# Performance work log

Measured on AMD Instinct MI355X. Metric: run time of the kernel, lower is better.

## Reference

```python
import jax, jax.numpy as jnp
import numpy as np

B, S, H, DK, DV, D = 1024, 8, 16, 32, 32, 512


def setup_inputs() -> dict:
    key = jax.random.key(0)
    ks = jax.random.split(key, 12)
    s = 1.0 / np.sqrt(D)
    return {
        "Q": jax.random.normal(ks[0], (B, S, D), jnp.float32),
        "K": jax.random.normal(ks[1], (B, S, D), jnp.float32),
        "V": jax.random.normal(ks[2], (B, S, D), jnp.float32),
        "attn_mask": jax.random.bernoulli(ks[3], 0.2, (B, S, S)),
        "hyper": jax.random.normal(ks[4], (B, H * S * DK), jnp.float32),
        "Wq": jax.random.normal(ks[5], (H * DK, D), jnp.float32) * s,
        "bq": jnp.zeros((H * DK,), jnp.float32),
        "Wk": jax.random.normal(ks[6], (H * DK, D), jnp.float32) * s,
        "bk": jnp.zeros((H * DK,), jnp.float32),
        "Wv": jax.random.normal(ks[7], (H * DV, D), jnp.float32) * s,
        "bv": jnp.zeros((H * DV,), jnp.float32),
        "Wo": jax.random.normal(ks[8], (D, H * DV), jnp.float32) * s,
        "bo": jnp.zeros((D,), jnp.float32),
        "ln_g": jnp.ones((D,), jnp.float32),
        "ln_b": jnp.zeros((D,), jnp.float32),
    }


def reference(Q, K, V, attn_mask, hyper, Wq, bq, Wk, bk, Wv, bv, Wo, bo, ln_g, ln_b):
    # QKV projections -> [B, H, S, dk]
    q = (Q @ Wq.T + bq).reshape(B, S, H, DK).transpose(0, 2, 1, 3)
    k = (K @ Wk.T + bk).reshape(B, S, H, DK).transpose(0, 2, 1, 3)
    v = (V @ Wv.T + bv).reshape(B, S, H, DV).transpose(0, 2, 1, 3)
    # scaled dot-product attention with mask
    scores = jnp.einsum('bhqd,bhkd->bhqk', q, k) / np.sqrt(DK).astype(np.float32)
    scores = jnp.where(attn_mask[:, None, :, :], -1e9, scores)
    weights = jax.nn.softmax(scores, axis=-1)
    # hyper-gated AV
    context = jnp.einsum('bhqk,bhkd->bhqd', weights, v) * hyper.reshape(B, H, S, DK)
    context = context.transpose(0, 2, 1, 3).reshape(B, S, H * DV)
    # output projection + residual layernorm (eps=1e-5)
    out = context @ Wo.T + bo + Q
    mu = out.mean(axis=-1, keepdims=True)
    var = out.var(axis=-1, keepdims=True)
    out = (out - mu) * jax.lax.rsqrt(var + 1e-5) * ln_g + ln_b
    return (out, weights)
```

## Files before the change

kernel.cpp:

```cpp
#include <hip/hip_runtime.h>
#include <hip/hip_bf16.h>
#include <cstdint>

#define NB 1024
#define ND 512
#define NM 8192

typedef __attribute__((ext_vector_type(8))) short short8;
typedef __attribute__((ext_vector_type(8))) __bf16 bf16x8;
typedef __attribute__((ext_vector_type(4))) float f32x4;
typedef __attribute__((ext_vector_type(4))) unsigned short ushort4v;

__device__ __forceinline__ unsigned short f2bf(float f) {
  uint32_t x = __builtin_bit_cast(uint32_t, f);
  x += 0x7fffu + ((x >> 16) & 1u);
  return (unsigned short)(x >> 16);
}
__device__ __forceinline__ float bf2f(unsigned short u) {
  return __builtin_bit_cast(float, (uint32_t)u << 16);
}
__device__ __forceinline__ f32x4 mfma16(short8 a, short8 b, f32x4 c) {
  return __builtin_amdgcn_mfma_f32_16x16x32_bf16(
      __builtin_bit_cast(bf16x8, a), __builtin_bit_cast(bf16x8, b), c, 0, 0, 0);
}

__global__ __launch_bounds__(256) void convert_w(
    const float* __restrict__ Wq, const float* __restrict__ Wk,
    const float* __restrict__ Wv, const float* __restrict__ Wo,
    unsigned short* __restrict__ Wqb, unsigned short* __restrict__ Wkb,
    unsigned short* __restrict__ Wvb, unsigned short* __restrict__ Wob) {
  const int idx = blockIdx.x * 256 + threadIdx.x;
  const int sel = idx >> 15, o = (idx & 32767) * 8;
  const float* src = sel == 0 ? Wq : sel == 1 ? Wk : sel == 2 ? Wv : Wo;
  unsigned short* dst = sel == 0 ? Wqb : sel == 1 ? Wkb : sel == 2 ? Wvb : Wob;
  const float4 a = ((const float4*)(src + o))[0];
  const float4 b = ((const float4*)(src + o))[1];
  short8 r;
  r[0] = (short)f2bf(a.x); r[1] = (short)f2bf(a.y);
  r[2] = (short)f2bf(a.z); r[3] = (short)f2bf(a.w);
  r[4] = (short)f2bf(b.x); r[5] = (short)f2bf(b.y);
  r[6] = (short)f2bf(b.z); r[7] = (short)f2bf(b.w);
  *(short8*)(dst + o) = r;
}

template <bool A_F32, int MODE>
__device__ __forceinline__ void gemm_tile(const void* __restrict__ A,
                                          const unsigned short* __restrict__ W,
                                          const float* __restrict__ bias,
                                          const float* __restrict__ resid,
                                          void* __restrict__ C, int mBase, int nBase) {
  __shared__ unsigned short As[128 * 64];
  __shared__ unsigned short Bs[128 * 64];
  const int tid = threadIdx.x;
  const int lane = tid & 63, wid = tid >> 6;
  const int wm = wid >> 2, wn = wid & 3;
  const int l15 = lane & 15, l4 = lane >> 4;
  f32x4 acc[4][2] = {};

  for (int kt = 0; kt < 8; ++kt) {
    const int kBase = kt * 64;
#pragma unroll
    for (int i = 0; i < 2; ++i) {
      const int Lb = i * 8192 + tid * 16;
      const int r = Lb >> 7;
      const int ce = (Lb & 127) >> 1;
      const int P = Lb ^ ((r & 7) << 4);
      short8 av;
      if (A_F32) {
        const float* src = (const float*)A + (size_t)(mBase + r) * ND + kBase + ce;
        const float4 a = ((const float4*)src)[0];
        const float4 b = ((const float4*)src)[1];
        av[0] = (short)f2bf(a.x); av[1] = (short)f2bf(a.y);
        av[2] = (short)f2bf(a.z); av[3] = (short)f2bf(a.w);
        av[4] = (short)f2bf(b.x); av[5] = (short)f2bf(b.y);
        av[6] = (short)f2bf(b.z); av[7] = (short)f2bf(b.w);
      } else {
        av = *(const short8*)((const unsigned short*)A +
                              (size_t)(mBase + r) * ND + kBase + ce);
      }
      const short8 wv = *(const short8*)(W + (size_t)(nBase + r) * ND + kBase + ce);
      *(short8*)((char*)As + P) = av;
      *(short8*)((char*)Bs + P) = wv;
    }
    __syncthreads();
#pragma unroll
    for (int kk = 0; kk < 2; ++kk) {
      short8 af[4], bf4[2];
#pragma unroll
      for (int m = 0; m < 4; ++m) {
        const int r = wm * 64 + m * 16 + l15;
        const int Lb = r * 128 + kk * 64 + l4 * 16;
        af[m] = *(const short8*)((char*)As + (Lb ^ ((r & 7) << 4)));
      }
#pragma unroll
      for (int n = 0; n < 2; ++n) {
        const int r = wn * 32 + n * 16 + l15;
        const int Lb = r * 128 + kk * 64 + l4 * 16;
        bf4[n] = *(const short8*)((char*)Bs + (Lb ^ ((r & 7) << 4)));
      }
#pragma unroll
      for (int m = 0; m < 4; ++m)
#pragma unroll
        for (int n = 0; n < 2; ++n)
          acc[m][n] = mfma16(af[m], bf4[n], acc[m][n]);
    }
    __syncthreads();
  }

#pragma unroll
  for (int m = 0; m < 4; ++m)
#pragma unroll
    for (int n = 0; n < 2; ++n) {
      const int gn = nBase + wn * 32 + n * 16 + l15;
      const float bb = bias ? bias[gn] : 0.f;
#pragma unroll
      for (int r4 = 0; r4 < 4; ++r4) {
        const int gm = mBase + wm * 64 + m * 16 + l4 * 4 + r4;
        float val = acc[m][n][r4] + bb;
        if (MODE == 0) {
          ((unsigned short*)C)[(size_t)gm * ND + gn] = f2bf(val);
        } else {
          val += resid[(size_t)gm * ND + gn];
          ((float*)C)[(size_t)gm * ND + gn] = val;
        }
      }
    }
}

__global__ __launch_bounds__(512) void gemm_qkv(
    const float* __restrict__ Q, const float* __restrict__ K,
    const float* __restrict__ V, const unsigned short* __restrict__ Wqb,
    const unsigned short* __restrict__ Wkb, const unsigned short* __restrict__ Wvb,
    const float* __restrict__ bq, const float* __restrict__ bk,
    const float* __restrict__ bv, unsigned short* __restrict__ qo,
    unsigned short* __restrict__ ko, unsigned short* __restrict__ vo) {
  const int bid = blockIdx.x;
  const int lid = (bid & 7) * 96 + (bid >> 3);
  const int by = lid / 12, bx = lid % 12;
  const int seg = bx >> 2, nloc = bx & 3;
  const float* A = seg == 0 ? Q : seg == 1 ? K : V;
  const unsigned short* W = seg == 0 ? Wqb : seg == 1 ? Wkb : Wvb;
  const float* bias = seg == 0 ? bq : seg == 1 ? bk : bv;
  unsigned short* C = seg == 0 ? qo : seg == 1 ? ko : vo;
  gemm_tile<true, 0>(A, W, bias, nullptr, C, by * 128, nloc * 128);
}

__global__ __launch_bounds__(512) void gemm_wo(const unsigned short* __restrict__ ctx,
                                               const unsigned short* __restrict__ Wob,
                                               const float* __restrict__ bo,
                                               const float* __restrict__ Qres,
                                               float* __restrict__ out) {
  const int bid = blockIdx.x;
  const int lid = (bid & 7) * 32 + (bid >> 3);
  const int by = lid >> 2, bx = lid & 3;
  gemm_tile<false, 1>(ctx, Wob, bo, Qres, out, by * 128, bx * 128);
}

__global__ __launch_bounds__(256) void attn_kernel(
    const unsigned short* __restrict__ q, const unsigned short* __restrict__ k,
    const unsigned short* __restrict__ v, const int* __restrict__ mask,
    const float* __restrict__ hyper, float* __restrict__ wout,
    unsigned short* __restrict__ ctx) {
  const int tid = threadIdx.x;
  const int wid = tid >> 6, lane = tid & 63;
  const int t = blockIdx.x * 4 + wid;
  const int b = t >> 4, h = t & 15;
  const int i = lane >> 3, j = lane & 7;

  const unsigned short* qrow = q + (size_t)(b * 8 + i) * ND + h * 32;
  const unsigned short* krow = k + (size_t)(b * 8 + j) * ND + h * 32;
  float dot = 0.f;
#pragma unroll
  for (int c = 0; c < 4; ++c) {
    const short8 qv = ((const short8*)qrow)[c];
    const short8 kv = ((const short8*)krow)[c];
#pragma unroll
    for (int e = 0; e < 8; ++e)
      dot += bf2f((unsigned short)qv[e]) * bf2f((unsigned short)kv[e]);
  }
  float score = dot * 0.17677669529663687f;
  if (mask[b * 64 + i * 8 + j]) score = -1e9f;

  float mx = score;
#pragma unroll
  for (int o = 4; o; o >>= 1) mx = fmaxf(mx, __shfl_xor(mx, o, 8));
  const float e = __expf(score - mx);
  float sm = e;
#pragma unroll
  for (int o = 4; o; o >>= 1) sm += __shfl_xor(sm, o, 8);
  const float w = e / sm;
  wout[(size_t)t * 64 + lane] = w;

  const int d0 = (lane & 7) * 4;
  float c0 = 0, c1 = 0, c2 = 0, c3 = 0;
#pragma unroll
  for (int jj = 0; jj < 8; ++jj) {
    const float wj = __shfl(w, jj, 8);
    const ushort4v vv = *(const ushort4v*)(v + (size_t)(b * 8 + jj) * ND + h * 32 + d0);
    c0 += wj * bf2f(vv[0]); c1 += wj * bf2f(vv[1]);
    c2 += wj * bf2f(vv[2]); c3 += wj * bf2f(vv[3]);
  }
  const float4 hv = *(const float4*)(hyper + (size_t)b * 4096 + h * 256 + i * 32 + d0);
  ushort4v co;
  co[0] = f2bf(c0 * hv.x); co[1] = f2bf(c1 * hv.y);
  co[2] = f2bf(c2 * hv.z); co[3] = f2bf(c3 * hv.w);
  *(ushort4v*)(ctx + (size_t)(b * 8 + i) * ND + h * 32 + d0) = co;
}

__global__ __launch_bounds__(256) void ln_kernel(float* __restrict__ io,
                                                 const float* __restrict__ g,
                                                 const float* __restrict__ be) {
  const int tid = threadIdx.x, wid = tid >> 6, lane = tid & 63;
  const size_t row = (size_t)blockIdx.x * 4 + wid;
  float* prow = io + row * ND + lane * 8;
  float4 x0 = ((float4*)prow)[0], x1 = ((float4*)prow)[1];
  float s = x0.x + x0.y + x0.z + x0.w + x1.x + x1.y + x1.z + x1.w;
  float sq = x0.x * x0.x + x0.y * x0.y + x0.z * x0.z + x0.w * x0.w +
             x1.x * x1.x + x1.y * x1.y + x1.z * x1.z + x1.w * x1.w;
#pragma unroll
  for (int o = 32; o; o >>= 1) {
    s += __shfl_xor(s, o, 64);
    sq += __shfl_xor(sq, o, 64);
  }
  const float mu = s * (1.f / 512.f);
  const float inv = rsqrtf(sq * (1.f / 512.f) - mu * mu + 1e-5f);
  const float4 g0 = ((const float4*)(g + lane * 8))[0];
  const float4 g1 = ((const float4*)(g + lane * 8))[1];
  const float4 e0 = ((const float4*)(be + lane * 8))[0];
  const float4 e1 = ((const float4*)(be + lane * 8))[1];
  float4 o0, o1;
  o0.x = (x0.x - mu) * inv * g0.x + e0.x; o0.y = (x0.y - mu) * inv * g0.y + e0.y;
  o0.z = (x0.z - mu) * inv * g0.z + e0.z; o0.w = (x0.w - mu) * inv * g0.w + e0.w;
  o1.x = (x1.x - mu) * inv * g1.x + e1.x; o1.y = (x1.y - mu) * inv * g1.y + e1.y;
  o1.z = (x1.z - mu) * inv * g1.z + e1.z; o1.w = (x1.w - mu) * inv * g1.w + e1.w;
  ((float4*)prow)[0] = o0;
  ((float4*)prow)[1] = o1;
}

extern "C" void kernel_launch(void* const* d_in, const int* in_sizes, int n_in,
                              void* d_out, int out_size, void* d_ws, size_t ws_size,
                              hipStream_t stream) {
  const float* Q = (const float*)d_in[0];
  const float* K = (const float*)d_in[1];
  const float* V = (const float*)d_in[2];
  const int* msk = (const int*)d_in[3];
  const float* hyper = (const float*)d_in[4];
  const float* Wq = (const float*)d_in[5];
  const float* bq = (const float*)d_in[6];
  const float* Wk = (const float*)d_in[7];
  const float* bk = (const float*)d_in[8];
  const float* Wv = (const float*)d_in[9];
  const float* bv = (const float*)d_in[10];
  const float* Wo = (const float*)d_in[11];
  const float* bo = (const float*)d_in[12];
  const float* lg = (const float*)d_in[13];
  const float* lb = (const float*)d_in[14];

  float* out = (float*)d_out;
  float* wout = out + (size_t)NM * ND;

  const size_t MAT = (size_t)NM * ND;
  unsigned short* qb = (unsigned short*)d_ws;
  unsigned short* kb = qb + MAT;
  unsigned short* vb = kb + MAT;
  unsigned short* ctxb = vb + MAT;
  unsigned short* Wqb = ctxb + MAT;
  unsigned short* Wkb = Wqb + (size_t)ND * ND;
  unsigned short* Wvb = Wkb + (size_t)ND * ND;
  unsigned short* Wob = Wvb + (size_t)ND * ND;

  convert_w<<<512, 256, 0, stream>>>(Wq, Wk, Wv, Wo, Wqb, Wkb, Wvb, Wob);
  gemm_qkv<<<768, 512, 0, stream>>>(Q, K, V, Wqb, Wkb, Wvb,
                                    bq, bk, bv, qb, kb, vb);
  attn_kernel<<<4096, 256, 0, stream>>>(qb, kb, vb, msk, hyper, wout, ctxb);
  gemm_wo<<<256, 512, 0, stream>>>(ctxb, Wob, bo, Q, out);
  ln_kernel<<<2048, 256, 0, stream>>>(out, lg, lb);
}
```

Measured before the change: 74.64 us.

## Prefetch next K-tile into registers during MFMA compute in GEMM tiles

```diff
diff --git a/kernel.cpp b/kernel.cpp
--- a/kernel.cpp
+++ b/kernel.cpp
@@ -43,6 +43,9 @@
   *(short8*)(dst + o) = r;
 }
 
+struct StageF32 { float4 a[4]; short8 w[2]; };
+struct StageBF  { short8 ab[2]; short8 w[2]; };
+
 template <bool A_F32, int MODE>
 __device__ __forceinline__ void gemm_tile(const void* __restrict__ A,
                                           const unsigned short* __restrict__ W,
@@ -55,34 +58,58 @@
   const int lane = tid & 63, wid = tid >> 6;
   const int wm = wid >> 2, wn = wid & 3;
   const int l15 = lane & 15, l4 = lane >> 4;
+  const int Lb0 = tid * 16, Lb1 = 8192 + tid * 16;
+  const int r0 = Lb0 >> 7, c0 = (Lb0 & 127) >> 1, P0 = Lb0 ^ ((r0 & 7) << 4);
+  const int r1 = Lb1 >> 7, c1 = (Lb1 & 127) >> 1, P1 = Lb1 ^ ((r1 & 7) << 4);
+
   f32x4 acc[4][2] = {};
-
+  StageF32 sf, nf;
+  StageBF sb, nb;
+
+  auto issue = [&](int kt, StageF32& f, StageBF& bfs) {
+    const int kBase = kt * 64;
+    if (A_F32) {
+      const float* s0 = (const float*)A + (size_t)(mBase + r0) * ND + kBase + c0;
+      const float* s1 = (const float*)A + (size_t)(mBase + r1) * ND + kBase + c1;
+      f.a[0] = ((const float4*)s0)[0]; f.a[1] = ((const float4*)s0)[1];
+      f.a[2] = ((const float4*)s1)[0]; f.a[3] = ((const float4*)s1)[1];
+      f.w[0] = *(const short8*)(W + (size_t)(nBase + r0) * ND + kBase + c0);
+      f.w[1] = *(const short8*)(W + (size_t)(nBase + r1) * ND + kBase + c1);
+    } else {
+      bfs.ab[0] = *(const short8*)((const unsigned short*)A + (size_t)(mBase + r0) * ND + kBase + c0);
+      bfs.ab[1] = *(const short8*)((const unsigned short*)A + (size_t)(mBase + r1) * ND + kBase + c1);
+      bfs.w[0] = *(const short8*)(W + (size_t)(nBase + r0) * ND + kBase + c0);
+      bfs.w[1] = *(const short8*)(W + (size_t)(nBase + r1) * ND + kBase + c1);
+    }
+  };
+  auto write_lds = [&](StageF32& f, StageBF& bfs) {
+    short8 av0, av1;
+    if (A_F32) {
+      av0[0] = (short)f2bf(f.a[0].x); av0[1] = (short)f2bf(f.a[0].y);
+      av0[2] = (short)f2bf(f.a[0].z); av0[3] = (short)f2bf(f.a[0].w);
+      av0[4] = (short)f2bf(f.a[1].x); av0[5] = (short)f2bf(f.a[1].y);
+      av0[6] = (short)f2bf(f.a[1].z); av0[7] = (short)f2bf(f.a[1].w);
+      av1[0] = (short)f2bf(f.a[2].x); av1[1] = (short)f2bf(f.a[2].y);
+      av1[2] = (short)f2bf(f.a[2].z); av1[3] = (short)f2bf(f.a[2].w);
+      av1[4] = (short)f2bf(f.a[3].x); av1[5] = (short)f2bf(f.a[3].y);
+      av1[6] = (short)f2bf(f.a[3].z); av1[7] = (short)f2bf(f.a[3].w);
+      *(short8*)((char*)As + P0) = av0;
+      *(short8*)((char*)As + P1) = av1;
+      *(short8*)((char*)Bs + P0) = f.w[0];
+      *(short8*)((char*)Bs + P1) = f.w[1];
+    } else {
+      *(short8*)((char*)As + P0) = bfs.ab[0];
+      *(short8*)((char*)As + P1) = bfs.ab[1];
+      *(short8*)((char*)Bs + P0) = bfs.w[0];
+      *(short8*)((char*)Bs + P1) = bfs.w[1];
+    }
+  };
+
+  issue(0, sf, sb);
   for (int kt = 0; kt < 8; ++kt) {
-    const int kBase = kt * 64;
-#pragma unroll
-    for (int i = 0; i < 2; ++i) {
-      const int Lb = i * 8192 + tid * 16;
-      const int r = Lb >> 7;
-      const int ce = (Lb & 127) >> 1;
-      const int P = Lb ^ ((r & 7) << 4);
-      short8 av;
-      if (A_F32) {
-        const float* src = (const float*)A + (size_t)(mBase + r) * ND + kBase + ce;
-        const float4 a = ((const float4*)src)[0];
-        const float4 b = ((const float4*)src)[1];
-        av[0] = (short)f2bf(a.x); av[1] = (short)f2bf(a.y);
-        av[2] = (short)f2bf(a.z); av[3] = (short)f2bf(a.w);
-        av[4] = (short)f2bf(b.x); av[5] = (short)f2bf(b.y);
-        av[6] = (short)f2bf(b.z); av[7] = (short)f2bf(b.w);
-      } else {
-        av = *(const short8*)((const unsigned short*)A +
-                              (size_t)(mBase + r) * ND + kBase + ce);
-      }
-      const short8 wv = *(const short8*)(W + (size_t)(nBase + r) * ND + kBase + ce);
-      *(short8*)((char*)As + P) = av;
-      *(short8*)((char*)Bs + P) = wv;
-    }
+    write_lds(sf, sb);
     __syncthreads();
+    if (kt < 7) issue(kt + 1, nf, nb);
 #pragma unroll
     for (int kk = 0; kk < 2; ++kk) {
       short8 af[4], bf4[2];
@@ -105,6 +132,8 @@
           acc[m][n] = mfma16(af[m], bf4[n], acc[m][n]);
     }
     __syncthreads();
+    sf = nf;
+    sb = nb;
   }
 
 #pragma unroll
@@ -127,7 +156,7 @@
     }
 }
 
-__global__ __launch_bounds__(512) void gemm_qkv(
+__global__ __launch_bounds__(512, 6) void gemm_qkv(
     const float* __restrict__ Q, const float* __restrict__ K,
     const float* __restrict__ V, const unsigned short* __restrict__ Wqb,
     const unsigned short* __restrict__ Wkb, const unsigned short* __restrict__ Wvb,
@@ -145,11 +174,11 @@
   gemm_tile<true, 0>(A, W, bias, nullptr, C, by * 128, nloc * 128);
 }
 
-__global__ __launch_bounds__(512) void gemm_wo(const unsigned short* __restrict__ ctx,
-                                               const unsigned short* __restrict__ Wob,
-                                               const float* __restrict__ bo,
-                                               const float* __restrict__ Qres,
-                                               float* __restrict__ out) {
+__global__ __launch_bounds__(512, 2) void gemm_wo(const unsigned short* __restrict__ ctx,
+                                                  const unsigned short* __restrict__ Wob,
+                                                  const float* __restrict__ bo,
+                                                  const float* __restrict__ Qres,
+                                                  float* __restrict__ out) {
   const int bid = blockIdx.x;
   const int lid = (bid & 7) * 32 + (bid >> 3);
   const int by = lid >> 2, bx = lid & 3;
```

Measured after the change: 72.97 us. -2.2%, faster.

## Use 256-wide K tiles with register-prefetched double staging in projection GEMMs

Applied to the files above, without the earlier changes.

```diff
diff --git a/kernel.cpp b/kernel.cpp
--- a/kernel.cpp
+++ b/kernel.cpp
@@ -44,58 +44,74 @@
 }
 
 template <bool A_F32, int MODE>
-__device__ __forceinline__ void gemm_tile(const void* __restrict__ A,
-                                          const unsigned short* __restrict__ W,
-                                          const float* __restrict__ bias,
-                                          const float* __restrict__ resid,
-                                          void* __restrict__ C, int mBase, int nBase) {
-  __shared__ unsigned short As[128 * 64];
-  __shared__ unsigned short Bs[128 * 64];
+__device__ __forceinline__ void gemm_big(const void* __restrict__ A,
+                                         const unsigned short* __restrict__ W,
+                                         const float* __restrict__ bias,
+                                         const float* __restrict__ resid,
+                                         void* __restrict__ C, int mBase, int nBase) {
+  __shared__ unsigned short As[128 * 256];
+  __shared__ unsigned short Bs[128 * 256];
   const int tid = threadIdx.x;
   const int lane = tid & 63, wid = tid >> 6;
   const int wm = wid >> 2, wn = wid & 3;
   const int l15 = lane & 15, l4 = lane >> 4;
+
   f32x4 acc[4][2] = {};
-
-  for (int kt = 0; kt < 8; ++kt) {
-    const int kBase = kt * 64;
-#pragma unroll
-    for (int i = 0; i < 2; ++i) {
-      const int Lb = i * 8192 + tid * 16;
-      const int r = Lb >> 7;
-      const int ce = (Lb & 127) >> 1;
+  float4 sa[16];
+  short8 sab[8];
+  short8 sw[8];
+
+  auto issue = [&](int kt) {
+    const int kBase = kt * 256;
+#pragma unroll
+    for (int j = 0; j < 8; ++j) {
+      const int Lb = j * 8192 + tid * 16;
+      const int r = Lb >> 9, ce = (Lb & 511) >> 1;
+      if (A_F32) {
+        const float* s = (const float*)A + (size_t)(mBase + r) * ND + kBase + ce;
+        sa[j * 2] = ((const float4*)s)[0];
+        sa[j * 2 + 1] = ((const float4*)s)[1];
+      } else {
+        sab[j] = *(const short8*)((const unsigned short*)A +
+                                  (size_t)(mBase + r) * ND + kBase + ce);
+      }
+      sw[j] = *(const short8*)(W + (size_t)(nBase + r) * ND + kBase + ce);
+    }
+  };
+  auto write_lds = [&]() {
+#pragma unroll
+    for (int j = 0; j < 8; ++j) {
+      const int Lb = j * 8192 + tid * 16;
+      const int r = Lb >> 9;
       const int P = Lb ^ ((r & 7) << 4);
-      short8 av;
       if (A_F32) {
-        const float* src = (const float*)A + (size_t)(mBase + r) * ND + kBase + ce;
-        const float4 a = ((const float4*)src)[0];
-        const float4 b = ((const float4*)src)[1];
-        av[0] = (short)f2bf(a.x); av[1] = (short)f2bf(a.y);
-        av[2] = (short)f2bf(a.z); av[3] = (short)f2bf(a.w);
-        av[4] = (short)f2bf(b.x); av[5] = (short)f2bf(b.y);
-        av[6] = (short)f2bf(b.z); av[7] = (short)f2bf(b.w);
+        short8 av;
+        const float4 a0 = sa[j * 2], a1 = sa[j * 2 + 1];
+        av[0] = (short)f2bf(a0.x); av[1] = (short)f2bf(a0.y);
+        av[2] = (short)f2bf(a0.z); av[3] = (short)f2bf(a0.w);
+        av[4] = (short)f2bf(a1.x); av[5] = (short)f2bf(a1.y);
+        av[6] = (short)f2bf(a1.z); av[7] = (short)f2bf(a1.w);
+        *(short8*)((char*)As + P) = av;
       } else {
-        av = *(const short8*)((const unsigned short*)A +
-                              (size_t)(mBase + r) * ND + kBase + ce);
-      }
-      const short8 wv = *(const short8*)(W + (size_t)(nBase + r) * ND + kBase + ce);
-      *(short8*)((char*)As + P) = av;
-      *(short8*)((char*)Bs + P) = wv;
+        *(short8*)((char*)As + P) = sab[j];
+      }
+      *(short8*)((char*)Bs + P) = sw[j];
     }
-    __syncthreads();
-#pragma unroll
-    for (int kk = 0; kk < 2; ++kk) {
+  };
+  auto compute = [&]() {
+#pragma unroll
+    for (int kk = 0; kk < 8; ++kk) {
       short8 af[4], bf4[2];
 #pragma unroll
       for (int m = 0; m < 4; ++m) {
         const int r = wm * 64 + m * 16 + l15;
-        const int Lb = r * 128 + kk * 64 + l4 * 16;
+        const int Lb = r * 512 + kk * 64 + l4 * 16;
         af[m] = *(const short8*)((char*)As + (Lb ^ ((r & 7) << 4)));
       }
 #pragma unroll
       for (int n = 0; n < 2; ++n) {
         const int r = wn * 32 + n * 16 + l15;
-        const int Lb = r * 128 + kk * 64 + l4 * 16;
+        const int Lb = r * 512 + kk * 64 + l4 * 16;
         bf4[n] = *(const short8*)((char*)Bs + (Lb ^ ((r & 7) << 4)));
       }
 #pragma unroll
@@ -104,8 +120,18 @@
         for (int n = 0; n < 2; ++n)
           acc[m][n] = mfma16(af[m], bf4[n], acc[m][n]);
     }
-    __syncthreads();
-  }
+  };
+
+  issue(0);
+  write_lds();
+  __syncthreads();
+  issue(1);
+  __builtin_amdgcn_sched_barrier(0);
+  compute();
+  __syncthreads();
+  write_lds();
+  __syncthreads();
+  compute();
 
 #pragma unroll
   for (int m = 0; m < 4; ++m)
@@ -127,7 +153,7 @@
     }
 }
 
-__global__ __launch_bounds__(512) void gemm_qkv(
+__global__ __launch_bounds__(512, 2) void gemm_qkv(
     const float* __restrict__ Q, const float* __restrict__ K,
     const float* __restrict__ V, const unsigned short* __restrict__ Wqb,
     const unsigned short* __restrict__ Wkb, const unsigned short* __restrict__ Wvb,
@@ -142,18 +168,18 @@
   const unsigned short* W = seg == 0 ? Wqb : seg == 1 ? Wkb : Wvb;
   const float* bias = seg == 0 ? bq : seg == 1 ? bk : bv;
   unsigned short* C = seg == 0 ? qo : seg == 1 ? ko : vo;
-  gemm_tile<true, 0>(A, W, bias, nullptr, C, by * 128, nloc * 128);
-}
-
-__global__ __launch_bounds__(512) void gemm_wo(const unsigned short* __restrict__ ctx,
-                                               const unsigned short* __restrict__ Wob,
-                                               const float* __restrict__ bo,
-                                               const float* __restrict__ Qres,
-                                               float* __restrict__ out) {
+  gemm_big<true, 0>(A, W, bias, nullptr, C, by * 128, nloc * 128);
+}
+
+__global__ __launch_bounds__(512, 2) void gemm_wo(const unsigned short* __restrict__ ctx,
+                                                  const unsigned short* __restrict__ Wob,
+                                                  const float* __restrict__ bo,
+                                                  const float* __restrict__ Qres,
+                                                  float* __restrict__ out) {
   const int bid = blockIdx.x;
   const int lid = (bid & 7) * 32 + (bid >> 3);
   const int by = lid >> 2, bx = lid & 3;
-  gemm_tile<false, 1>(ctx, Wob, bo, Qres, out, by * 128, bx * 128);
+  gemm_big<false, 1>(ctx, Wob, bo, Qres, out, by * 128, bx * 128);
 }
 
 __global__ __launch_bounds__(256) void attn_kernel(
```

Result: slower. 80.63 us (+8.0%).

## Replace LDS-tiled GEMMs with register-direct MFMA loads and larger per-wave tiles

Applied to the files above, without the earlier changes.

```diff
diff --git a/kernel.cpp b/kernel.cpp
--- a/kernel.cpp
+++ b/kernel.cpp
@@ -22,6 +22,14 @@
 __device__ __forceinline__ f32x4 mfma16(short8 a, short8 b, f32x4 c) {
   return __builtin_amdgcn_mfma_f32_16x16x32_bf16(
       __builtin_bit_cast(bf16x8, a), __builtin_bit_cast(bf16x8, b), c, 0, 0, 0);
+}
+__device__ __forceinline__ short8 cvt8(float4 a, float4 b) {
+  short8 r;
+  r[0] = (short)f2bf(a.x); r[1] = (short)f2bf(a.y);
+  r[2] = (short)f2bf(a.z); r[3] = (short)f2bf(a.w);
+  r[4] = (short)f2bf(b.x); r[5] = (short)f2bf(b.y);
+  r[6] = (short)f2bf(b.z); r[7] = (short)f2bf(b.w);
+  return r;
 }
 
 __global__ __launch_bounds__(256) void convert_w(
@@ -35,125 +43,157 @@
   unsigned short* dst = sel == 0 ? Wqb : sel == 1 ? Wkb : sel == 2 ? Wvb : Wob;
   const float4 a = ((const float4*)(src + o))[0];
   const float4 b = ((const float4*)(src + o))[1];
-  short8 r;
-  r[0] = (short)f2bf(a.x); r[1] = (short)f2bf(a.y);
-  r[2] = (short)f2bf(a.z); r[3] = (short)f2bf(a.w);
-  r[4] = (short)f2bf(b.x); r[5] = (short)f2bf(b.y);
-  r[6] = (short)f2bf(b.z); r[7] = (short)f2bf(b.w);
-  *(short8*)(dst + o) = r;
-}
-
-template <bool A_F32, int MODE>
-__device__ __forceinline__ void gemm_tile(const void* __restrict__ A,
-                                          const unsigned short* __restrict__ W,
-                                          const float* __restrict__ bias,
-                                          const float* __restrict__ resid,
-                                          void* __restrict__ C, int mBase, int nBase) {
-  __shared__ unsigned short As[128 * 64];
-  __shared__ unsigned short Bs[128 * 64];
-  const int tid = threadIdx.x;
-  const int lane = tid & 63, wid = tid >> 6;
-  const int wm = wid >> 2, wn = wid & 3;
-  const int l15 = lane & 15, l4 = lane >> 4;
-  f32x4 acc[4][2] = {};
-
-  for (int kt = 0; kt < 8; ++kt) {
-    const int kBase = kt * 64;
-#pragma unroll
-    for (int i = 0; i < 2; ++i) {
-      const int Lb = i * 8192 + tid * 16;
-      const int r = Lb >> 7;
-      const int ce = (Lb & 127) >> 1;
-      const int P = Lb ^ ((r & 7) << 4);
-      short8 av;
-      if (A_F32) {
-        const float* src = (const float*)A + (size_t)(mBase + r) * ND + kBase + ce;
-        const float4 a = ((const float4*)src)[0];
-        const float4 b = ((const float4*)src)[1];
-        av[0] = (short)f2bf(a.x); av[1] = (short)f2bf(a.y);
-        av[2] = (short)f2bf(a.z); av[3] = (short)f2bf(a.w);
-        av[4] = (short)f2bf(b.x); av[5] = (short)f2bf(b.y);
-        av[6] = (short)f2bf(b.z); av[7] = (short)f2bf(b.w);
-      } else {
-        av = *(const short8*)((const unsigned short*)A +
-                              (size_t)(mBase + r) * ND + kBase + ce);
-      }
-      const short8 wv = *(const short8*)(W + (size_t)(nBase + r) * ND + kBase + ce);
-      *(short8*)((char*)As + P) = av;
-      *(short8*)((char*)Bs + P) = wv;
-    }
-    __syncthreads();
-#pragma unroll
-    for (int kk = 0; kk < 2; ++kk) {
-      short8 af[4], bf4[2];
-#pragma unroll
-      for (int m = 0; m < 4; ++m) {
-        const int r = wm * 64 + m * 16 + l15;
-        const int Lb = r * 128 + kk * 64 + l4 * 16;
-        af[m] = *(const short8*)((char*)As + (Lb ^ ((r & 7) << 4)));
-      }
-#pragma unroll
-      for (int n = 0; n < 2; ++n) {
-        const int r = wn * 32 + n * 16 + l15;
-        const int Lb = r * 128 + kk * 64 + l4 * 16;
-        bf4[n] = *(const short8*)((char*)Bs + (Lb ^ ((r & 7) << 4)));
-      }
-#pragma unroll
-      for (int m = 0; m < 4; ++m)
-#pragma unroll
-        for (int n = 0; n < 2; ++n)
-          acc[m][n] = mfma16(af[m], bf4[n], acc[m][n]);
-    }
-    __syncthreads();
-  }
-
-#pragma unroll
-  for (int m = 0; m < 4; ++m)
-#pragma unroll
-    for (int n = 0; n < 2; ++n) {
-      const int gn = nBase + wn * 32 + n * 16 + l15;
-      const float bb = bias ? bias[gn] : 0.f;
-#pragma unroll
-      for (int r4 = 0; r4 < 4; ++r4) {
-        const int gm = mBase + wm * 64 + m * 16 + l4 * 4 + r4;
-        float val = acc[m][n][r4] + bb;
-        if (MODE == 0) {
-          ((unsigned short*)C)[(size_t)gm * ND + gn] = f2bf(val);
-        } else {
-          val += resid[(size_t)gm * ND + gn];
-          ((float*)C)[(size_t)gm * ND + gn] = val;
-        }
-      }
-    }
-}
-
-__global__ __launch_bounds__(512) void gemm_qkv(
-    const float* __restrict__ Q, const float* __restrict__ K,
-    const float* __restrict__ V, const unsigned short* __restrict__ Wqb,
-    const unsigned short* __restrict__ Wkb, const unsigned short* __restrict__ Wvb,
+  *(short8*)(dst + o) = cvt8(a, b);
+}
+
+__global__ __launch_bounds__(256, 2) void gemm_qkv(
+    const float* __restrict__ Qf, const float* __restrict__ Kf,
+    const float* __restrict__ Vf,
+    const unsigned short* __restrict__ Wqb, const unsigned short* __restrict__ Wkb,
+    const unsigned short* __restrict__ Wvb,
     const float* __restrict__ bq, const float* __restrict__ bk,
-    const float* __restrict__ bv, unsigned short* __restrict__ qo,
-    unsigned short* __restrict__ ko, unsigned short* __restrict__ vo) {
+    const float* __restrict__ bv,
+    unsigned short* __restrict__ qo, unsigned short* __restrict__ ko,
+    unsigned short* __restrict__ vo) {
   const int bid = blockIdx.x;
-  const int lid = (bid & 7) * 96 + (bid >> 3);
-  const int by = lid / 12, bx = lid % 12;
-  const int seg = bx >> 2, nloc = bx & 3;
-  const float* A = seg == 0 ? Q : seg == 1 ? K : V;
+  const int lid = (bid & 7) * 48 + (bid >> 3);
+  const int mgrp = lid / 12, nb = lid % 12;
+  const int seg = nb >> 2, nloc = nb & 3;
+  const float* A = seg == 0 ? Qf : seg == 1 ? Kf : Vf;
   const unsigned short* W = seg == 0 ? Wqb : seg == 1 ? Wkb : Wvb;
   const float* bias = seg == 0 ? bq : seg == 1 ? bk : bv;
   unsigned short* C = seg == 0 ? qo : seg == 1 ? ko : vo;
-  gemm_tile<true, 0>(A, W, bias, nullptr, C, by * 128, nloc * 128);
-}
-
-__global__ __launch_bounds__(512) void gemm_wo(const unsigned short* __restrict__ ctx,
-                                               const unsigned short* __restrict__ Wob,
-                                               const float* __restrict__ bo,
-                                               const float* __restrict__ Qres,
-                                               float* __restrict__ out) {
+
+  const int tid = threadIdx.x, lane = tid & 63, wid = tid >> 6;
+  const int l15 = lane & 15, l4 = lane >> 4;
+  const int mBase = mgrp * 256 + wid * 64;
+  const int nBase = nloc * 128;
+
+  const float* Arow[4];
+  const unsigned short* Wrow[8];
+#pragma unroll
+  for (int mf = 0; mf < 4; ++mf)
+    Arow[mf] = A + (size_t)(mBase + mf * 16 + l15) * ND + l4 * 8;
+#pragma unroll
+  for (int nf = 0; nf < 8; ++nf)
+    Wrow[nf] = W + (size_t)(nBase + nf * 16 + l15) * ND + l4 * 8;
+
+  f32x4 acc[4][8] = {};
+  float4 a0[4][2];
+#pragma unroll
+  for (int mf = 0; mf < 4; ++mf) {
+    a0[mf][0] = ((const float4*)Arow[mf])[0];
+    a0[mf][1] = ((const float4*)Arow[mf])[1];
+  }
+
+  for (int kt = 0; kt < 16; ++kt) {
+    short8 bfr[8];
+#pragma unroll
+    for (int nf = 0; nf < 8; ++nf)
+      bfr[nf] = *(const short8*)(Wrow[nf] + kt * 32);
+    short8 af[4];
+#pragma unroll
+    for (int mf = 0; mf < 4; ++mf) af[mf] = cvt8(a0[mf][0], a0[mf][1]);
+    if (kt < 15) {
+#pragma unroll
+      for (int mf = 0; mf < 4; ++mf) {
+        a0[mf][0] = ((const float4*)(Arow[mf] + (kt + 1) * 32))[0];
+        a0[mf][1] = ((const float4*)(Arow[mf] + (kt + 1) * 32))[1];
+      }
+    }
+#pragma unroll
+    for (int mf = 0; mf < 4; ++mf)
+#pragma unroll
+      for (int nf = 0; nf < 8; ++nf)
+        acc[mf][nf] = mfma16(af[mf], bfr[nf], acc[mf][nf]);
+  }
+
+#pragma unroll
+  for (int nf = 0; nf < 8; ++nf) {
+    const int gn = nBase + nf * 16 + l15;
+    const float bb = bias[gn];
+#pragma unroll
+    for (int mf = 0; mf < 4; ++mf)
+#pragma unroll
+      for (int r = 0; r < 4; ++r) {
+        const int gm = mBase + mf * 16 + l4 * 4 + r;
+        C[(size_t)gm * ND + gn] = f2bf(acc[mf][nf][r] + bb);
+      }
+  }
+}
+
+__global__ __launch_bounds__(256, 2) void gemm_wo(
+    const unsigned short* __restrict__ ctx, const unsigned short* __restrict__ Wob,
+    const float* __restrict__ bo, const float* __restrict__ Qres,
+    float* __restrict__ out) {
   const int bid = blockIdx.x;
-  const int lid = (bid & 7) * 32 + (bid >> 3);
-  const int by = lid >> 2, bx = lid & 3;
-  gemm_tile<false, 1>(ctx, Wob, bo, Qres, out, by * 128, bx * 128);
+  const int lid = (bid & 7) * 16 + (bid >> 3);
+  const int mgrp = lid >> 2, nloc = lid & 3;
+  const int tid = threadIdx.x, lane = tid & 63, wid = tid >> 6;
+  const int l15 = lane & 15, l4 = lane >> 4;
+  const int mBase = mgrp * 256 + wid * 64;
+  const int nBase = nloc * 128;
+
+  const unsigned short* Arow[4];
+  const unsigned short* Wrow[8];
+#pragma unroll
+  for (int mf = 0; mf < 4; ++mf)
+    Arow[mf] = ctx + (size_t)(mBase + mf * 16 + l15) * ND + l4 * 8;
+#pragma unroll
+  for (int nf = 0; nf < 8; ++nf)
+    Wrow[nf] = Wob + (size_t)(nBase + nf * 16 + l15) * ND + l4 * 8;
+
+  f32x4 acc[4][8] = {};
+  short8 aA[4], aB[4];
+#pragma unroll
+  for (int mf = 0; mf < 4; ++mf) aA[mf] = *(const short8*)Arow[mf];
+
+  for (int kt = 0; kt < 16; kt += 2) {
+#pragma unroll
+    for (int mf = 0; mf < 4; ++mf)
+      aB[mf] = *(const short8*)(Arow[mf] + (kt + 1) * 32);
+    {
+      short8 bfr[8];
+#pragma unroll
+      for (int nf = 0; nf < 8; ++nf)
+        bfr[nf] = *(const short8*)(Wrow[nf] + kt * 32);
+#pragma unroll
+      for (int mf = 0; mf < 4; ++mf)
+#pragma unroll
+        for (int nf = 0; nf < 8; ++nf)
+          acc[mf][nf] = mfma16(aA[mf], bfr[nf], acc[mf][nf]);
+    }
+    if (kt + 2 < 16) {
+#pragma unroll
+      for (int mf = 0; mf < 4; ++mf)
+        aA[mf] = *(const short8*)(Arow[mf] + (kt + 2) * 32);
+    }
+    {
+      short8 bfr[8];
+#pragma unroll
+      for (int nf = 0; nf < 8; ++nf)
+        bfr[nf] = *(const short8*)(Wrow[nf] + (kt + 1) * 32);
+#pragma unroll
+      for (int mf = 0; mf < 4; ++mf)
+#pragma unroll
+        for (int nf = 0; nf < 8; ++nf)
+          acc[mf][nf] = mfma16(aB[mf], bfr[nf], acc[mf][nf]);
+    }
+  }
+
+#pragma unroll
+  for (int nf = 0; nf < 8; ++nf) {
+    const int gn = nBase + nf * 16 + l15;
+    const float bb = bo[gn];
+#pragma unroll
+    for (int mf = 0; mf < 4; ++mf)
+#pragma unroll
+      for (int r = 0; r < 4; ++r) {
+        const int gm = mBase + mf * 16 + l4 * 4 + r;
+        out[(size_t)gm * ND + gn] =
+            acc[mf][nf][r] + bb + Qres[(size_t)gm * ND + gn];
+      }
+  }
 }
 
 __global__ __launch_bounds__(256) void attn_kernel(
@@ -270,9 +310,9 @@
   unsigned short* Wob = Wvb + (size_t)ND * ND;
 
   convert_w<<<512, 256, 0, stream>>>(Wq, Wk, Wv, Wo, Wqb, Wkb, Wvb, Wob);
-  gemm_qkv<<<768, 512, 0, stream>>>(Q, K, V, Wqb, Wkb, Wvb,
+  gemm_qkv<<<384, 256, 0, stream>>>(Q, K, V, Wqb, Wkb, Wvb,
                                     bq, bk, bv, qb, kb, vb);
   attn_kernel<<<4096, 256, 0, stream>>>(qb, kb, vb, msk, hyper, wout, ctxb);
-  gemm_wo<<<256, 512, 0, stream>>>(ctxb, Wob, bo, Q, out);
+  gemm_wo<<<128, 256, 0, stream>>>(ctxb, Wob, bo, Q, out);
   ln_kernel<<<2048, 256, 0, stream>>>(out, lg, lb);
 }
```

Result: slower. 151.5 us (+103.0%).
